# Performance work log

Hardware: AMD Instinct MI355X
Metric: run time of the kernel (lower is better)

## Reference

```python
import jax, jax.numpy as jnp
import numpy as np

TEMP = 0.5
PATCH = 8
EPS = 1e-05


def _to_patches(x, h, w):
    # [B,C,H,W] -> [B*PATCH*PATCH, h*w, C], patch order (b, j, k) row-major
    B, C, H, W = x.shape
    x = x.reshape(B, C, PATCH, h, PATCH, w)
    x = x.transpose(0, 2, 4, 3, 5, 1)  # B, j, k, h, w, C
    return x.reshape(B * PATCH * PATCH, h * w, C)


def setup_inputs() -> dict:
    key = jax.random.key(0)
    k1, k2, k3, k4, k5 = jax.random.split(key, 5)
    B, C, H, W, L = 8, 256, 64, 64, 32
    return {
        "main_out": jax.random.normal(k1, (B, C, H, W), dtype=jnp.float32),
        "ema_out": jax.random.normal(k2, (B, C, H, W), dtype=jnp.float32),
        "main_label": jax.random.uniform(k3, (B, 4 * H, 4 * W), dtype=jnp.float32),
        "neg_banks": jax.random.normal(k4, (L, C, H // PATCH, W // PATCH), dtype=jnp.float32),
        "pos_banks": jax.random.normal(k5, (L, C, H // PATCH, W // PATCH), dtype=jnp.float32),
    }


def reference(main_out, ema_out, main_label, neg_banks, pos_banks):
    B, C, H, W = main_out.shape
    h, w = H // PATCH, W // PATCH
    hh, ww = 4 * h, 4 * w

    anchors = _to_patches(main_out, h, w)      # [BP, hw, C]
    pos_pair = _to_patches(ema_out, h, w)      # [BP, hw, C]

    neg_flat = neg_banks.transpose(0, 2, 3, 1).reshape(-1, C)  # [L*h*w, C]
    pos_flat = pos_banks.transpose(0, 2, 3, 1).reshape(-1, C)

    # per-patch mean of label, order (b, j, k) matching _to_patches
    lab = main_label.reshape(B, PATCH, hh, PATCH, ww).mean(axis=(2, 4))  # [B,8,8]
    use_pos = (lab.reshape(-1) < 0.1)[:, None, None]  # [BP,1,1]

    sim_neg = jnp.einsum("pnc,mc->pnm", anchors, neg_flat) / TEMP
    sim_posbank = jnp.einsum("pnc,mc->pnm", anchors, pos_flat) / TEMP
    neg_sim = jnp.where(use_pos, sim_posbank, sim_neg)  # [BP, hw, M]

    pos_sim = (anchors * pos_pair).sum(-1, keepdims=True) / TEMP  # [BP, hw, 1]

    allsim = jnp.concatenate([pos_sim, neg_sim], axis=-1)
    m = allsim.max(axis=-1, keepdims=True)
    denom = jnp.exp(allsim - m).sum(-1) + EPS            # [BP, hw]
    frac = jnp.exp(pos_sim - m)[..., 0] / denom
    loss_patch = -jnp.log(frac + EPS)                    # [BP, hw]
    # sum of per-patch means divided by B*PATCH^2 == global mean (equal patch sizes)
    return loss_patch.mean()
```

## Files before the change

### kernel.cpp

```cpp
#include <hip/hip_runtime.h>

typedef __attribute__((ext_vector_type(4))) float f32x4;
typedef __attribute__((ext_vector_type(4))) int i32x4;
typedef __attribute__((ext_vector_type(8))) int i32x8;

#define EPSV 1e-5f
#define SCALE 2.885390081777927f

__device__ __forceinline__ float fast_exp2(float x) { return __builtin_amdgcn_exp2f(x); }

__device__ __forceinline__ unsigned f32_to_fp4(float v) {
  const float m = fabsf(v);
  unsigned c = (unsigned)(m > 0.25f) + (unsigned)(m > 0.75f) + (unsigned)(m > 1.25f)
             + (unsigned)(m > 1.75f) + (unsigned)(m > 2.5f)  + (unsigned)(m > 3.5f)
             + (unsigned)(m > 5.0f);
  return c | (v < 0.f ? 8u : 0u);
}

__device__ __forceinline__ i32x8 pad4(i32x4 p) {
  i32x8 r; r[0] = p[0]; r[1] = p[1]; r[2] = p[2]; r[3] = p[3];
  r[4] = 0; r[5] = 0; r[6] = 0; r[7] = 0;
  return r;
}

__device__ __forceinline__ void dma16(const void* g, void* l) {
  __builtin_amdgcn_global_load_lds(
      (const __attribute__((address_space(1))) unsigned*)g,
      (__attribute__((address_space(3))) unsigned*)l, 16, 0, 0);
}


__global__ __launch_bounds__(256) void cpl_prep(
    const float* __restrict__ mainO, const float* __restrict__ emaO,
    const float* __restrict__ label, const float* __restrict__ negB,
    const float* __restrict__ posB,
    unsigned char* __restrict__ Apk, float* __restrict__ posDot,
    int* __restrict__ flags, unsigned char* __restrict__ bankN,
    unsigned char* __restrict__ bankP)
{
  __shared__ __align__(16) unsigned char shU[64 * 256];
  __shared__ float shF[4][64];
  const int bid = blockIdx.x;
  const int t = threadIdx.x;

  if (bid < 512) {
    const int b = bid >> 6, y = bid & 63;
    const int cg = t >> 4;
    const int x4 = t & 15;
    const float* mB = mainO + (((size_t)b * 256 + cg) * 64 + y) * 64 + x4 * 4;
    const float* eB = emaO  + (((size_t)b * 256 + cg) * 64 + y) * 64 + x4 * 4;
    float4 acc4 = make_float4(0.f, 0.f, 0.f, 0.f);
#pragma unroll
    for (int pass = 0; pass < 16; ++pass) {
      const int c = pass * 16 + cg;
      const float4 mv = *(const float4*)(mB + (size_t)pass * 16 * 4096);
      const float4 ev = *(const float4*)(eB + (size_t)pass * 16 * 4096);
      acc4.x += mv.x * ev.x; acc4.y += mv.y * ev.y;
      acc4.z += mv.z * ev.z; acc4.w += mv.w * ev.w;
      const float vals[4] = {mv.x, mv.y, mv.z, mv.w};
#pragma unroll
      for (int j = 0; j < 4; ++j) {
        const int x = x4 * 4 + j;
        shU[x * 256 + (c ^ ((x & 7) << 4))] = (unsigned char)f32_to_fp4(vals[j]);
      }
    }
    acc4.x += __shfl_xor(acc4.x, 16, 64); acc4.y += __shfl_xor(acc4.y, 16, 64);
    acc4.z += __shfl_xor(acc4.z, 16, 64); acc4.w += __shfl_xor(acc4.w, 16, 64);
    acc4.x += __shfl_xor(acc4.x, 32, 64); acc4.y += __shfl_xor(acc4.y, 32, 64);
    acc4.z += __shfl_xor(acc4.z, 32, 64); acc4.w += __shfl_xor(acc4.w, 32, 64);
    if ((t & 63) < 16) *(float4*)&shF[t >> 6][(t & 15) * 4] = acc4;
    __syncthreads();
#pragma unroll
    for (int it = 0; it < 2; ++it) {
      const int ch = it * 256 + t;
      const int x = ch >> 3, rem = ch & 7;
      const int kq = rem >> 2, kg = rem & 3;
      const int swz = (x & 7) << 4;
      unsigned wrd[4];
#pragma unroll
      for (int w4 = 0; w4 < 4; ++w4) {
        unsigned v = 0;
#pragma unroll
        for (int k = 0; k < 4; ++k) {
          const int bo = w4 * 4 + k;
          const int c0 = kq * 128 + kg * 32 + 2 * bo;
          const unsigned lo = shU[x * 256 + (c0 ^ swz)];
          const unsigned hi = shU[x * 256 + ((c0 + 1) ^ swz)];
          v |= ((lo | (hi << 4)) & 0xffu) << (8 * k);
        }
        wrd[w4] = v;
      }
      const int p = b * 64 + ((y >> 3) << 3) + (x >> 3);
      const int n = ((y & 7) << 3) + (x & 7);
      const int mt = n >> 4, r16n = n & 15;
      uint4 o; o.x = wrd[0]; o.y = wrd[1]; o.z = wrd[2]; o.w = wrd[3];
      *(uint4*)&Apk[(size_t)p * 8192 + mt * 2048 + kq * 1024 + kg * 256 + r16n * 16] = o;
    }
    if (t < 64) {
      const float pv = shF[0][t] + shF[1][t] + shF[2][t] + shF[3][t];
      const int p = b * 64 + ((y >> 3) << 3) + (t >> 3);
      const int n = ((y & 7) << 3) + (t & 7);
      posDot[p * 64 + n] = pv;
    }
  } else if (bid < 1024) {
    const int p = bid - 512;
    const int b = p >> 6, pj = (p >> 3) & 7, pk = p & 7;
    const size_t base = ((size_t)b * 256 + pj * 32) * 256 + pk * 32;
    float s = 0.f;
#pragma unroll
    for (int i = 0; i < 4; ++i) {
      const int e = t * 4 + i;
      s += label[base + (size_t)(e >> 5) * 256 + (e & 31)];
    }
#pragma unroll
    for (int d = 1; d < 64; d <<= 1) s += __shfl_xor(s, d, 64);
    if ((t & 63) == 0) shF[0][t >> 6] = s;
    __syncthreads();
    if (t == 0)
      flags[p] = ((shF[0][0] + shF[0][1] + shF[0][2] + shF[0][3]) * (1.f / 1024.f) < 0.1f) ? 1 : 0;
  } else {
    const int bb = bid - 1024;
    const float* src = (bb < 32 ? negB : posB) + (size_t)(bb & 31) * 16384;
    unsigned char* dst = (bb < 32 ? bankN : bankP) + (size_t)(bb & 31) * 8192;
#pragma unroll 8
    for (int it = 0; it < 64; ++it) {
      const int lin = it * 256 + t;
      const int c = lin >> 6, posi = lin & 63;
      shU[posi * 256 + (c ^ ((posi & 7) << 3))] = (unsigned char)f32_to_fp4(src[lin]);
    }
    __syncthreads();
#pragma unroll
    for (int it = 0; it < 2; ++it) {
      const int ch = it * 256 + t;
      const int ct = ch >> 7, kq = (ch >> 6) & 1, kb = (ch >> 4) & 3, col = ch & 15;
      const int posi = ct * 16 + col;
      const int swz = (posi & 7) << 3;
      const int cb = kq * 128 + kb * 32;
      unsigned wrd[4];
#pragma unroll
      for (int w4 = 0; w4 < 4; ++w4) {
        unsigned v = 0;
#pragma unroll
        for (int k = 0; k < 4; ++k) {
          const int bo = w4 * 4 + k;
          const unsigned lo = shU[posi * 256 + ((cb + 2 * bo) ^ swz)];
          const unsigned hi = shU[posi * 256 + ((cb + 2 * bo + 1) ^ swz)];
          v |= ((lo | (hi << 4)) & 0xffu) << (8 * k);
        }
        wrd[w4] = v;
      }
      uint4 o; o.x = wrd[0]; o.y = wrd[1]; o.z = wrd[2]; o.w = wrd[3];
      *(uint4*)&dst[ct * 2048 + kq * 1024 + kb * 256 + col * 16] = o;
    }
  }
}

__global__ __launch_bounds__(256, 2) void cpl_main(
    const unsigned char* __restrict__ Apk, const float* __restrict__ posDot,
    const unsigned char* __restrict__ bankN, const unsigned char* __restrict__ bankP,
    const int* __restrict__ flags, float* __restrict__ blockSums)
{
  __shared__ __align__(1024) unsigned char Bsm[4 * 8 * 2048];
  __shared__ float swS[4][64];

  const int p = blockIdx.x;
  const int t = threadIdx.x;
  const int l = t & 63, w = t >> 6;
  const int r16 = l & 15, kg = l >> 4;
  const int qph = (p * 11) & 31;

  const unsigned char* bankB = flags[p] ? bankP : bankN;
  const unsigned char* wsrc = bankB + (size_t)w * 65536;
  unsigned char* wlds = Bsm + w * 16384;
  const int dmaOfs = l * 16;

  const unsigned char* Ab = Apk + (size_t)p * 8192;
  i32x8 afrag[4][2];
#pragma unroll
  for (int mt = 0; mt < 4; ++mt)
#pragma unroll
    for (int kq = 0; kq < 2; ++kq)
      afrag[mt][kq] = pad4(*(const i32x4*)(Ab + mt * 2048 + kq * 1024 + kg * 256 + r16 * 16));
#pragma unroll
  for (int mt = 0; mt < 4; ++mt)
#pragma unroll
    for (int kq = 0; kq < 2; ++kq)
      asm volatile("" : "+v"(afrag[mt][kq]));

  f32x4 negS[4];
#pragma unroll
  for (int mt = 0; mt < 4; ++mt) {
    f32x4 v = *(const f32x4*)(posDot + (size_t)p * 64 + mt * 16 + kg * 4);
#pragma unroll
    for (int i = 0; i < 4; ++i) negS[mt][i] = -v[i] * SCALE;
  }
#pragma unroll
  for (int mt = 0; mt < 4; ++mt) asm volatile("" : "+v"(negS[mt]));

  asm volatile("s_waitcnt vmcnt(0)" ::: "memory");

#define ISSUEQ(TT, SLOT) do {                                                      \
    const unsigned char* g_ = wsrc + (size_t)((((TT) + qph) & 31)) * 2048 + dmaOfs;\
    unsigned char* l_ = wlds + (SLOT) * 2048;                                      \
    dma16(g_, l_);                                                                 \
    dma16(g_ + 1024, l_ + 1024);                                                   \
  } while (0)

  float s[16];
#pragma unroll
  for (int e = 0; e < 16; ++e) s[e] = 0.f;

  f32x4 acc[4];
  const f32x4 zeroC = {0.f, 0.f, 0.f, 0.f};
  const unsigned char* rbase = wlds + kg * 256 + r16 * 16;

#define MFMA_TILE(PB0, PB1) do {                                                   \
    const i32x8 b0_ = pad4(PB0);                                                   \
    _Pragma("unroll") for (int mt = 0; mt < 4; ++mt)                               \
      acc[mt] = __builtin_amdgcn_mfma_scale_f32_16x16x128_f8f6f4(                  \
          afrag[mt][0], b0_, zeroC, 4, 4, 0, 127, 0, 127);                         \
    const i32x8 b1_ = pad4(PB1);                                                   \
    _Pragma("unroll") for (int mt = 0; mt < 4; ++mt)                               \
      acc[mt] = __builtin_amdgcn_mfma_scale_f32_16x16x128_f8f6f4(                  \
          afrag[mt][1], b1_, acc[mt], 4, 4, 0, 127, 0, 127);                       \
  } while (0)

#define EXPACC() do {                                                              \
    _Pragma("unroll") for (int mt = 0; mt < 4; ++mt)                               \
      _Pragma("unroll") for (int i = 0; i < 4; ++i)                                \
        s[mt * 4 + i] += fast_exp2(__builtin_fmaf(acc[mt][i], SCALE,               \
                                                  negS[mt][i])); } while (0)

#define STEP(TT, SLOT, DO_ISSUE, WN) do {                                          \
    asm volatile("s_waitcnt vmcnt(" #WN ")" ::: "memory");                         \
    __builtin_amdgcn_sched_barrier(0);                                             \
    if (DO_ISSUE) ISSUEQ((TT) + 7, ((SLOT) + 7) & 7);                              \
    { const unsigned char* rb_ = rbase + (SLOT) * 2048;                            \
      i32x4 P0 = *(const i32x4*)rb_;                                               \
      i32x4 P1 = *(const i32x4*)(rb_ + 1024);                                      \
      __builtin_amdgcn_s_setprio(1);                                               \
      MFMA_TILE(P0, P1);                                                           \
      __builtin_amdgcn_s_setprio(0); }                                             \
    EXPACC();                                                                      \
    __builtin_amdgcn_sched_barrier(0);                                             \
  } while (0)

  ISSUEQ(0, 0); ISSUEQ(1, 1); ISSUEQ(2, 2); ISSUEQ(3, 3);
  ISSUEQ(4, 4); ISSUEQ(5, 5); ISSUEQ(6, 6);

  for (int g = 0; g < 3; ++g) {
    const int n0 = g * 8;
    STEP(n0 + 0, 0, 1, 12);
    STEP(n0 + 1, 1, 1, 12);
    STEP(n0 + 2, 2, 1, 12);
    STEP(n0 + 3, 3, 1, 12);
    STEP(n0 + 4, 4, 1, 12);
    STEP(n0 + 5, 5, 1, 12);
    STEP(n0 + 6, 6, 1, 12);
    STEP(n0 + 7, 7, 1, 12);
  }
  STEP(24, 0, 1, 12);
  STEP(25, 1, 0, 12);
  STEP(26, 2, 0, 10);
  STEP(27, 3, 0,  8);
  STEP(28, 4, 0,  6);
  STEP(29, 5, 0,  4);
  STEP(30, 6, 0,  2);
  STEP(31, 7, 0,  0);

#undef STEP
#undef EXPACC
#undef MFMA_TILE
#undef ISSUEQ

#pragma unroll
  for (int d = 1; d < 16; d <<= 1)
#pragma unroll
    for (int e = 0; e < 16; ++e) s[e] += __shfl_xor(s[e], d, 64);
  if (r16 == 0) {
#pragma unroll
    for (int mt = 0; mt < 4; ++mt)
#pragma unroll
      for (int i = 0; i < 4; ++i)
        swS[w][mt * 16 + kg * 4 + i] = s[mt * 4 + i];
  }
  __syncthreads();

  if (t < 64) {
    const float S = 1.f + swS[0][t] + swS[1][t] + swS[2][t] + swS[3][t];
    float loss = -logf(1.f / S + EPSV);
#pragma unroll
    for (int d = 1; d < 64; d <<= 1) loss += __shfl_xor(loss, d, 64);
    if (t == 0) blockSums[p] = loss;
  }
}

__global__ void cpl_final(const float* __restrict__ blockSums, float* __restrict__ out) {
  const int t = threadIdx.x;
  float s = blockSums[t] + blockSums[t + 256];
#pragma unroll
  for (int d = 1; d < 64; d <<= 1) s += __shfl_xor(s, d, 64);
  __shared__ float ps[4];
  if ((t & 63) == 0) ps[t >> 6] = s;
  __syncthreads();
  if (t == 0) out[0] = (ps[0] + ps[1] + ps[2] + ps[3]) * (1.f / 32768.f);
}

extern "C" void kernel_launch(void* const* d_in, const int* in_sizes, int n_in,
                              void* d_out, int out_size, void* d_ws, size_t ws_size,
                              hipStream_t stream) {
  const float* mainO = (const float*)d_in[0];
  const float* emaO  = (const float*)d_in[1];
  const float* label = (const float*)d_in[2];
  const float* negB  = (const float*)d_in[3];
  const float* posB  = (const float*)d_in[4];
  float* out = (float*)d_out;

  char* ws = (char*)d_ws;
  float*         blockSums = (float*)ws;
  int*           flags     = (int*)(ws + 2048);
  unsigned char* bankN     = (unsigned char*)(ws + 4096);
  unsigned char* bankP     = (unsigned char*)(ws + 266240);
  float*         posDot    = (float*)(ws + 528384);
  unsigned char* Apk       = (unsigned char*)(ws + 659456);

  hipLaunchKernelGGL(cpl_prep, dim3(1088), dim3(256), 0, stream,
                     mainO, emaO, label, negB, posB, Apk, posDot, flags, bankN, bankP);
  hipLaunchKernelGGL(cpl_main, dim3(512), dim3(256), 0, stream,
                     Apk, posDot, bankN, bankP, flags, blockSums);
  hipLaunchKernelGGL(cpl_final, dim3(1), dim3(256), 0, stream, blockSums, out);
}
```

Measured before the change: 39.89 us.

## Deepen bank prefetch ring to nine slots and fuse final reduction via atomics

Each wave's LDS ring for streamed bank tiles grows from eight to nine slots, so eight tiles stay in flight instead of seven, giving more latency hiding at the cost of more LDS per block. The separate single-block final reduction kernel is removed. Each main block instead atomically adds its loss to a global accumulator, and the last block, found with a ticket counter, writes the mean. This removes one kernel launch but makes the float summation order nondeterministic.

```diff
diff --git a/kernel.cpp b/kernel.cpp
--- a/kernel.cpp
+++ b/kernel.cpp
@@ -36,7 +36,8 @@
     const float* __restrict__ posB,
     unsigned char* __restrict__ Apk, float* __restrict__ posDot,
     int* __restrict__ flags, unsigned char* __restrict__ bankN,
-    unsigned char* __restrict__ bankP)
+    unsigned char* __restrict__ bankP, float* __restrict__ accum,
+    unsigned* __restrict__ ticket)
 {
   __shared__ __align__(16) unsigned char shU[64 * 256];
   __shared__ float shF[4][64];
@@ -104,6 +105,7 @@
     }
   } else if (bid < 1024) {
     const int p = bid - 512;
+    if (p == 0 && t == 0) { *accum = 0.f; *ticket = 0u; }
     const int b = p >> 6, pj = (p >> 3) & 7, pk = p & 7;
     const size_t base = ((size_t)b * 256 + pj * 32) * 256 + pk * 32;
     float s = 0.f;
@@ -158,9 +160,10 @@
 __global__ __launch_bounds__(256, 2) void cpl_main(
     const unsigned char* __restrict__ Apk, const float* __restrict__ posDot,
     const unsigned char* __restrict__ bankN, const unsigned char* __restrict__ bankP,
-    const int* __restrict__ flags, float* __restrict__ blockSums)
+    const int* __restrict__ flags, float* __restrict__ accum,
+    unsigned* __restrict__ ticket, float* __restrict__ out)
 {
-  __shared__ __align__(1024) unsigned char Bsm[4 * 8 * 2048];
+  __shared__ __align__(1024) unsigned char Bsm[4 * 9 * 2048];
   __shared__ float swS[4][64];
 
   const int p = blockIdx.x;
@@ -171,7 +174,7 @@
 
   const unsigned char* bankB = flags[p] ? bankP : bankN;
   const unsigned char* wsrc = bankB + (size_t)w * 65536;
-  unsigned char* wlds = Bsm + w * 16384;
+  unsigned char* wlds = Bsm + w * 18432;
   const int dmaOfs = l * 16;
 
   const unsigned char* Ab = Apk + (size_t)p * 8192;
@@ -231,10 +234,10 @@
         s[mt * 4 + i] += fast_exp2(__builtin_fmaf(acc[mt][i], SCALE,               \
                                                   negS[mt][i])); } while (0)
 
-#define STEP(TT, SLOT, DO_ISSUE, WN) do {                                          \
+#define STEP(TT, SLOT, DO_ISSUE, ISLOT, WN) do {                                   \
     asm volatile("s_waitcnt vmcnt(" #WN ")" ::: "memory");                         \
     __builtin_amdgcn_sched_barrier(0);                                             \
-    if (DO_ISSUE) ISSUEQ((TT) + 7, ((SLOT) + 7) & 7);                              \
+    if (DO_ISSUE) ISSUEQ((TT) + 8, ISLOT);                                         \
     { const unsigned char* rb_ = rbase + (SLOT) * 2048;                            \
       i32x4 P0 = *(const i32x4*)rb_;                                               \
       i32x4 P1 = *(const i32x4*)(rb_ + 1024);                                      \
@@ -246,27 +249,19 @@
   } while (0)
 
   ISSUEQ(0, 0); ISSUEQ(1, 1); ISSUEQ(2, 2); ISSUEQ(3, 3);
-  ISSUEQ(4, 4); ISSUEQ(5, 5); ISSUEQ(6, 6);
-
-  for (int g = 0; g < 3; ++g) {
-    const int n0 = g * 8;
-    STEP(n0 + 0, 0, 1, 12);
-    STEP(n0 + 1, 1, 1, 12);
-    STEP(n0 + 2, 2, 1, 12);
-    STEP(n0 + 3, 3, 1, 12);
-    STEP(n0 + 4, 4, 1, 12);
-    STEP(n0 + 5, 5, 1, 12);
-    STEP(n0 + 6, 6, 1, 12);
-    STEP(n0 + 7, 7, 1, 12);
-  }
-  STEP(24, 0, 1, 12);
-  STEP(25, 1, 0, 12);
-  STEP(26, 2, 0, 10);
-  STEP(27, 3, 0,  8);
-  STEP(28, 4, 0,  6);
-  STEP(29, 5, 0,  4);
-  STEP(30, 6, 0,  2);
-  STEP(31, 7, 0,  0);
+  ISSUEQ(4, 4); ISSUEQ(5, 5); ISSUEQ(6, 6); ISSUEQ(7, 7);
+
+  STEP( 0, 0, 1, 8, 14);  STEP( 1, 1, 1, 0, 14);  STEP( 2, 2, 1, 1, 14);
+  STEP( 3, 3, 1, 2, 14);  STEP( 4, 4, 1, 3, 14);  STEP( 5, 5, 1, 4, 14);
+  STEP( 6, 6, 1, 5, 14);  STEP( 7, 7, 1, 6, 14);  STEP( 8, 8, 1, 7, 14);
+  STEP( 9, 0, 1, 8, 14);  STEP(10, 1, 1, 0, 14);  STEP(11, 2, 1, 1, 14);
+  STEP(12, 3, 1, 2, 14);  STEP(13, 4, 1, 3, 14);  STEP(14, 5, 1, 4, 14);
+  STEP(15, 6, 1, 5, 14);  STEP(16, 7, 1, 6, 14);  STEP(17, 8, 1, 7, 14);
+  STEP(18, 0, 1, 8, 14);  STEP(19, 1, 1, 0, 14);  STEP(20, 2, 1, 1, 14);
+  STEP(21, 3, 1, 2, 14);  STEP(22, 4, 1, 3, 14);  STEP(23, 5, 1, 4, 14);
+  STEP(24, 6, 0, 0, 14);  STEP(25, 7, 0, 0, 12);  STEP(26, 8, 0, 0, 10);
+  STEP(27, 0, 0, 0,  8);  STEP(28, 1, 0, 0,  6);  STEP(29, 2, 0, 0,  4);
+  STEP(30, 3, 0, 0,  2);  STEP(31, 4, 0, 0,  0);
 
 #undef STEP
 #undef EXPACC
@@ -291,19 +286,17 @@
     float loss = -logf(1.f / S + EPSV);
 #pragma unroll
     for (int d = 1; d < 64; d <<= 1) loss += __shfl_xor(loss, d, 64);
-    if (t == 0) blockSums[p] = loss;
+    if (t == 0) {
+      atomicAdd(accum, loss);
+      __threadfence();
+      const unsigned old = atomicAdd(ticket, 1u);
+      if (old == 511u) {
+        __threadfence();
+        const float tot = atomicAdd(accum, 0.f);
+        out[0] = tot * (1.f / 32768.f);
+      }
+    }
   }
-}
-
-__global__ void cpl_final(const float* __restrict__ blockSums, float* __restrict__ out) {
-  const int t = threadIdx.x;
-  float s = blockSums[t] + blockSums[t + 256];
-#pragma unroll
-  for (int d = 1; d < 64; d <<= 1) s += __shfl_xor(s, d, 64);
-  __shared__ float ps[4];
-  if ((t & 63) == 0) ps[t >> 6] = s;
-  __syncthreads();
-  if (t == 0) out[0] = (ps[0] + ps[1] + ps[2] + ps[3]) * (1.f / 32768.f);
 }
 
 extern "C" void kernel_launch(void* const* d_in, const int* in_sizes, int n_in,
@@ -317,16 +310,17 @@
   float* out = (float*)d_out;
 
   char* ws = (char*)d_ws;
-  float*         blockSums = (float*)ws;
-  int*           flags     = (int*)(ws + 2048);
-  unsigned char* bankN     = (unsigned char*)(ws + 4096);
-  unsigned char* bankP     = (unsigned char*)(ws + 266240);
-  float*         posDot    = (float*)(ws + 528384);
-  unsigned char* Apk       = (unsigned char*)(ws + 659456);
+  float*         accum  = (float*)ws;
+  unsigned*      ticket = (unsigned*)(ws + 4);
+  int*           flags  = (int*)(ws + 2048);
+  unsigned char* bankN  = (unsigned char*)(ws + 4096);
+  unsigned char* bankP  = (unsigned char*)(ws + 266240);
+  float*         posDot = (float*)(ws + 528384);
+  unsigned char* Apk    = (unsigned char*)(ws + 659456);
 
   hipLaunchKernelGGL(cpl_prep, dim3(1088), dim3(256), 0, stream,
-                     mainO, emaO, label, negB, posB, Apk, posDot, flags, bankN, bankP);
+                     mainO, emaO, label, negB, posB, Apk, posDot, flags,
+                     bankN, bankP, accum, ticket);
   hipLaunchKernelGGL(cpl_main, dim3(512), dim3(256), 0, stream,
-                     Apk, posDot, bankN, bankP, flags, blockSums);
-  hipLaunchKernelGGL(cpl_final, dim3(1), dim3(256), 0, stream, blockSums, out);
-}
+                     Apk, posDot, bankN, bankP, flags, accum, ticket, out);
+}
```

Result: slower. 51.21 us (+28.4%).
